# Optimization experiments

Hardware: AMD Instinct MI355X
Metric: run time of the kernel (lower is better)

The kernel has to match this reference:

```python
import jax, jax.numpy as jnp
import numpy as np

B, N, D, H, DH = 1, 1024, 512, 16, 32
NBINS, KIT = 68, 20
NEG = jnp.float32(-1e9)


def _ln(x, g, b):
    mu = jnp.mean(x, -1, keepdims=True)
    var = jnp.mean((x - mu) ** 2, -1, keepdims=True)
    return (x - mu) * jax.lax.rsqrt(var + 1e-5) * g + b


def _heads(x, W):
    b, n, _ = x.shape
    return (x @ W).reshape(b, n, H, DH).transpose(0, 2, 1, 3)  # (B,H,N,DH)


def _forward(h, x_res, pos_bins, mask, ln_mha_g, ln_mha_b, w_q, w_k, w_v, w_g, w_o,
             pos_w, ln_ff_g, ln_ff_b, sw_w1, sw_w3, sw_w2, ln_sink_g, ln_sink_b,
             w_q_sink, w_k_sink, alpha_h, r_h, eps, ln_gate_g, ln_gate_b,
             w_gate_w, w_gate_b, lambda_h_raw):
    b, n, d = h.shape
    mcol = mask[:, None, None, :] > 0  # key-side mask (B,1,1,N)
    mrow = mask[:, None, :, None] > 0

    # ---- MHA with positional bias (flash_diff_attn reference math) ----
    h_n = _ln(h, ln_mha_g, ln_mha_b)
    Q = _heads(h_n, w_q)
    K = _heads(h_n, w_k)
    V = _heads(h_n, w_v)
    G = h_n @ w_g  # (B,N,D) gate, per-head view is equivalent flattened
    bias = pos_w[pos_bins].transpose(0, 3, 1, 2)  # (B,N,N,H) -> (B,H,N,N)
    logits = jnp.einsum('bhnd,bhmd->bhnm', Q, K) / np.float32(np.sqrt(DH)) + bias
    logits = jnp.where(mcol, logits, NEG)
    P = jax.nn.softmax(logits, axis=-1)
    att = jnp.einsum('bhnm,bhmd->bhnd', P, V).transpose(0, 2, 1, 3).reshape(b, n, d)
    h = h + jax.nn.sigmoid(G) * (att @ w_o) * mask[..., None]

    # ---- SwiGLU FFN ----
    h_f = _ln(h, ln_ff_g, ln_ff_b)
    ff = (jax.nn.silu(h_f @ sw_w1) * (h_f @ sw_w3)) @ sw_w2
    h = h + ff * mask[..., None]

    # ---- Balanced Sinkhorn OT transport over coordinates ----
    h_s = _ln(h, ln_sink_g, ln_sink_b)
    Qs = _heads(h_s, w_q_sink)
    Ks = _heads(h_s, w_k_sink)
    Qs = Qs / jnp.clip(jnp.linalg.norm(Qs, axis=-1, keepdims=True), 1e-12)
    Ks = Ks / jnp.clip(jnp.linalg.norm(Ks, axis=-1, keepdims=True), 1e-12)
    sim = jnp.einsum('bhnd,bhmd->bhnm', Qs, Ks)  # cosine similarity
    # Gibbs log-kernel: higher (r_h*sim + alpha_h) => lower cost, scaled by per-head eps
    logKmat = (r_h[:, None, None] * sim + alpha_h[:, None, None]) / eps[:, None, None]
    logKmat = jnp.where(mcol, logKmat, NEG)
    logKmat = jnp.where(mrow, logKmat, NEG)
    n_valid = jnp.sum(mask, -1, keepdims=True)  # (B,1)
    log_a = jnp.where(mask > 0, -jnp.log(n_valid), NEG)[:, None, :]  # (B,1,N) uniform marginal

    def sink_step(carry, _):
        f, g = carry
        f = log_a - jax.nn.logsumexp(logKmat + g[..., None, :], axis=-1)
        g = log_a - jax.nn.logsumexp(logKmat + f[..., None], axis=-2)
        return (f, g), None

    f0 = jnp.zeros((b, H, n), h.dtype)
    (f, g), _ = jax.lax.scan(sink_step, (f0, f0), None, length=KIT)
    logP = f[..., None] + logKmat + g[..., None, :]
    Pn = jax.nn.softmax(logP, axis=-1)  # barycentric row-normalized plan
    x_cent = jnp.einsum('bhnm,bmc->bhnc', Pn, x_res)  # (B,H,N,3)
    vec_h = x_cent - x_res[:, None]

    gate = jax.nn.sigmoid(_ln(h, ln_gate_g, ln_gate_b) @ w_gate_w + w_gate_b)  # (B,N,1)
    lam = (jnp.tanh(lambda_h_raw) / H).reshape(1, H, 1, 1)
    disp = jnp.sum(lam * vec_h, axis=1)  # (B,N,3)
    x_out = x_res + gate * disp * mask[..., None]
    return h, x_out


def setup_inputs() -> dict:
    key = jax.random.key(0)
    ks = jax.random.split(key, 16)
    w = lambda k, s: (0.02 * jax.random.normal(k, s)).astype(jnp.float32)
    nr = H // 4
    return {
        'h': jax.random.normal(ks[0], (B, N, D), jnp.float32),
        'x_res': jax.random.normal(ks[1], (B, N, 3), jnp.float32),
        'pos_bins': jax.random.randint(ks[2], (B, N, N), 0, NBINS),
        'mask': jnp.ones((B, N), jnp.float32),
        'ln_mha_g': jnp.ones(D), 'ln_mha_b': jnp.zeros(D),
        'w_q': w(ks[3], (D, D)), 'w_k': w(ks[4], (D, D)), 'w_v': w(ks[5], (D, D)),
        'w_g': w(ks[6], (D, D)), 'w_o': w(ks[7], (D, D)),
        'pos_w': w(ks[8], (NBINS, H)),
        'ln_ff_g': jnp.ones(D), 'ln_ff_b': jnp.zeros(D),
        'sw_w1': w(ks[9], (D, 4 * D)), 'sw_w3': w(ks[10], (D, 4 * D)),
        'sw_w2': w(ks[11], (4 * D, D)),
        'ln_sink_g': jnp.ones(D), 'ln_sink_b': jnp.zeros(D),
        'w_q_sink': w(ks[12], (D, D)), 'w_k_sink': w(ks[13], (D, D)),
        'alpha_h': jnp.full((H,), -1.0, jnp.float32),
        'r_h': jnp.full((H,), 10.0, jnp.float32),
        'eps': jnp.asarray([0.5] * nr + [1.0] * nr + [2.0] * nr + [4.0] * nr, jnp.float32),
        'ln_gate_g': jnp.ones(D), 'ln_gate_b': jnp.zeros(D),
        'w_gate_w': w(ks[14], (D, 1)), 'w_gate_b': jnp.zeros(1),
        'lambda_h_raw': jnp.zeros(H, jnp.float32),
    }


def reference(h, x_res, pos_bins, mask, ln_mha_g, ln_mha_b, w_q, w_k, w_v, w_g, w_o,
              pos_w, ln_ff_g, ln_ff_b, sw_w1, sw_w3, sw_w2, ln_sink_g, ln_sink_b,
              w_q_sink, w_k_sink, alpha_h, r_h, eps, ln_gate_g, ln_gate_b,
              w_gate_w, w_gate_b, lambda_h_raw):
    return _forward(h, x_res, pos_bins, mask, ln_mha_g, ln_mha_b, w_q, w_k, w_v, w_g,
                    w_o, pos_w, ln_ff_g, ln_ff_b, sw_w1, sw_w3, sw_w2, ln_sink_g,
                    ln_sink_b, w_q_sink, w_k_sink, alpha_h, r_h, eps, ln_gate_g,
                    ln_gate_b, w_gate_w, w_gate_b, lambda_h_raw)
```

## Files before the change

### kernel.cpp

```cpp
#include <hip/hip_runtime.h>
#include <hip/hip_bf16.h>
#include <hip/hip_fp16.h>
#include <math.h>

#define NTOK 1024
#define DMODEL 512
#define NHEAD 16
#define DHEAD 32
#define DFF 2048
#define NBINS 68
#define KIT 20
#define NEGV (-1e9f)
#define NEGH (-30000.0f)

typedef __attribute__((ext_vector_type(8))) short bf16x8;
typedef __attribute__((ext_vector_type(4))) float f32x4;
typedef __attribute__((ext_vector_type(8))) unsigned short u16x8;

__device__ inline unsigned short f2bf(float f) {
    unsigned int u = __float_as_uint(f);
    unsigned int r = (u + 0x7fff + ((u >> 16) & 1)) >> 16;
    return (unsigned short)r;
}

__device__ inline float wave_max64(float v) {
    #pragma unroll
    for (int s = 32; s; s >>= 1) v = fmaxf(v, __shfl_xor(v, s, 64));
    return v;
}
__device__ inline float wave_sum64(float v) {
    #pragma unroll
    for (int s = 32; s; s >>= 1) v += __shfl_xor(v, s, 64);
    return v;
}

__global__ void prep_kernel(const float* __restrict__ w_q, const float* __restrict__ w_k,
                            const float* __restrict__ w_v, const float* __restrict__ w_g,
                            const float* __restrict__ w_o, const float* __restrict__ w_qs,
                            const float* __restrict__ w_ks, const float* __restrict__ sw1,
                            const float* __restrict__ sw3, const float* __restrict__ sw2,
                            unsigned short* __restrict__ wt_qkvg, unsigned short* __restrict__ wt_o,
                            unsigned short* __restrict__ wt_qsks, unsigned short* __restrict__ wt_13,
                            unsigned short* __restrict__ wt_2,
                            const float* __restrict__ mask, float* __restrict__ la,
                            float* __restrict__ gv,
                            const float* __restrict__ hin, const float* __restrict__ lng,
                            const float* __restrict__ lnb, unsigned short* __restrict__ hnb) {
    __shared__ float red[256];
    __shared__ float T[32][33];
    int b = blockIdx.x, tid = threadIdx.x;
    if (b == 4864) {
        red[tid] = mask[tid] + mask[tid + 256] + mask[tid + 512] + mask[tid + 768];
        __syncthreads();
        for (int off = 128; off; off >>= 1) { if (tid < off) red[tid] += red[tid + off]; __syncthreads(); }
        float lognv = __logf(red[0]);
        for (int i = tid; i < NTOK; i += 256) la[i] = (mask[i] > 0.f) ? -lognv : NEGV;
        for (int i = tid; i < NHEAD * NTOK; i += 256)
            gv[i] = (mask[i & 1023] > 0.f) ? 0.f : NEGV;
        return;
    }
    if (b > 4864) {
        int n = b - 4865;
        const float* row = hin + (size_t)n * DMODEL;
        float a = row[tid], bb = row[tid + 256];
        red[tid] = a + bb;
        __syncthreads();
        for (int off = 128; off; off >>= 1) { if (tid < off) red[tid] += red[tid + off]; __syncthreads(); }
        float mu = red[0] * (1.0f / DMODEL);
        __syncthreads();
        float d0 = a - mu, d1 = bb - mu;
        red[tid] = d0 * d0 + d1 * d1;
        __syncthreads();
        for (int off = 128; off; off >>= 1) { if (tid < off) red[tid] += red[tid + off]; __syncthreads(); }
        float rstd = rsqrtf(red[0] * (1.0f / DMODEL) + 1e-5f);
        hnb[(size_t)n * DMODEL + tid]       = f2bf(d0 * rstd * lng[tid] + lnb[tid]);
        hnb[(size_t)n * DMODEL + tid + 256] = f2bf(d1 * rstd * lng[tid + 256] + lnb[tid + 256]);
        return;
    }
    const float* W; unsigned short* D; int K, N, t;
    if (b < 1792) {
        int which = b >> 8; t = b & 255; K = 512; N = 512;
        switch (which) {
            case 0: W = w_q;  D = wt_qkvg; break;
            case 1: W = w_k;  D = wt_qkvg + 512 * 512; break;
            case 2: W = w_v;  D = wt_qkvg + 2 * 512 * 512; break;
            case 3: W = w_g;  D = wt_qkvg + 3 * 512 * 512; break;
            case 4: W = w_o;  D = wt_o; break;
            case 5: W = w_qs; D = wt_qsks; break;
            default: W = w_ks; D = wt_qsks + 512 * 512; break;
        }
    } else if (b < 2816) { W = sw1; D = wt_13;              K = 512;  N = 2048; t = b - 1792; }
    else if (b < 3840)   { W = sw3; D = wt_13 + 2048 * 512; K = 512;  N = 2048; t = b - 2816; }
    else                 { W = sw2; D = wt_2;               K = 2048; N = 512;  t = b - 3840; }
    int nx = N >> 5;
    int n0 = (t % nx) * 32, k0 = (t / nx) * 32;
    int r = tid >> 3, c0 = (tid & 7) * 4;
    float4 v4 = *(const float4*)&W[(size_t)(k0 + r) * N + n0 + c0];
    T[r][c0] = v4.x; T[r][c0 + 1] = v4.y; T[r][c0 + 2] = v4.z; T[r][c0 + 3] = v4.w;
    __syncthreads();
    ushort4 o;
    o.x = f2bf(T[c0][r]); o.y = f2bf(T[c0 + 1][r]);
    o.z = f2bf(T[c0 + 2][r]); o.w = f2bf(T[c0 + 3][r]);
    *(ushort4*)&D[(size_t)(n0 + r) * K + k0 + c0] = o;
}

template<int GATED>
__global__ void res_ln_kernel(const float* __restrict__ base, const __half* __restrict__ Gh,
                              const float* __restrict__ t1, const float* __restrict__ mask,
                              const float* __restrict__ gm, const float* __restrict__ bt,
                              float* __restrict__ hout, unsigned short* __restrict__ lnout) {
    int n = blockIdx.x, tid = threadIdx.x;
    __shared__ float red[256];
    float mk = mask[n];
    size_t off = (size_t)n * DMODEL;
    float a, b;
    if (GATED) {
        float g0 = __half2float(Gh[off + tid]);
        float g1 = __half2float(Gh[off + tid + 256]);
        a = base[off + tid]       + g0 * t1[off + tid]       * mk;
        b = base[off + tid + 256] + g1 * t1[off + tid + 256] * mk;
    } else {
        a = base[off + tid]       + t1[off + tid]       * mk;
        b = base[off + tid + 256] + t1[off + tid + 256] * mk;
    }
    hout[off + tid] = a; hout[off + tid + 256] = b;
    red[tid] = a + b;
    __syncthreads();
    for (int o2 = 128; o2; o2 >>= 1) { if (tid < o2) red[tid] += red[tid + o2]; __syncthreads(); }
    float mu = red[0] * (1.0f / DMODEL);
    __syncthreads();
    float d0 = a - mu, d1 = b - mu;
    red[tid] = d0 * d0 + d1 * d1;
    __syncthreads();
    for (int o2 = 128; o2; o2 >>= 1) { if (tid < o2) red[tid] += red[tid + o2]; __syncthreads(); }
    float rstd = rsqrtf(red[0] * (1.0f / DMODEL) + 1e-5f);
    lnout[off + tid]       = f2bf(d0 * rstd * gm[tid] + bt[tid]);
    lnout[off + tid + 256] = f2bf(d1 * rstd * gm[tid + 256] + bt[tid + 256]);
}

template<int MODE>
__global__ __launch_bounds__(256)
void mfma_gemm(const unsigned short* __restrict__ A, const unsigned short* __restrict__ Bt,
               float* __restrict__ C, __half* __restrict__ Ch, unsigned short* __restrict__ Cb,
               unsigned short* __restrict__ P2, unsigned short* __restrict__ P3,
               int N, int K, int lda, int ldb, int ldc,
               long sA, long sB, long sC) {
    __shared__ unsigned short As[128 * 64];
    __shared__ unsigned short Bs[128 * 64];
    int h = blockIdx.z;
    A += (size_t)h * sA; Bt += (size_t)h * sB;
    const int tid = threadIdx.x;
    const int lane = tid & 63, wid = tid >> 6;
    const int wr = wid >> 1, wc = wid & 1;
    const int lr = lane & 15, kg = lane >> 4;
    const int row0 = blockIdx.y * 128, col0 = blockIdx.x * 128;
    f32x4 acc[4][4];
    #pragma unroll
    for (int i = 0; i < 4; i++)
        #pragma unroll
        for (int j = 0; j < 4; j++) acc[i][j] = (f32x4){0.f, 0.f, 0.f, 0.f};

    for (int k0 = 0; k0 < K; k0 += 64) {
        #pragma unroll
        for (int i = 0; i < 4; i++) {
            int cid = tid + i * 256;
            int r = cid >> 3, sl = cid & 7;
            int rb = col0 + r; if (rb > N - 1) rb = N - 1;
            u16x8 va = *(const u16x8*)&A[(size_t)(row0 + r) * lda + k0 + sl * 8];
            u16x8 vb = *(const u16x8*)&Bt[(size_t)rb * ldb + k0 + sl * 8];
            *(u16x8*)&As[r * 64 + ((sl ^ (r & 7)) * 8)] = va;
            *(u16x8*)&Bs[r * 64 + ((sl ^ (r & 7)) * 8)] = vb;
        }
        __syncthreads();
        #pragma unroll
        for (int ks = 0; ks < 2; ks++) {
            bf16x8 af[4], bfr[4];
            #pragma unroll
            for (int f = 0; f < 4; f++) {
                int ra = wr * 64 + f * 16 + lr;
                af[f] = *(const bf16x8*)&As[ra * 64 + (((ks * 4 + kg) ^ (ra & 7)) * 8)];
                int rb = wc * 64 + f * 16 + lr;
                bfr[f] = *(const bf16x8*)&Bs[rb * 64 + (((ks * 4 + kg) ^ (rb & 7)) * 8)];
            }
            #pragma unroll
            for (int i = 0; i < 4; i++)
                #pragma unroll
                for (int j = 0; j < 4; j++)
                    acc[i][j] = __builtin_amdgcn_mfma_f32_16x16x32_bf16(af[i], bfr[j], acc[i][j], 0, 0, 0);
        }
        __syncthreads();
    }
    #pragma unroll
    for (int i = 0; i < 4; i++) {
        int row = row0 + wr * 64 + i * 16 + kg * 4;
        #pragma unroll
        for (int j = 0; j < 4; j++) {
            int col = col0 + wc * 64 + j * 16 + lr;
            #pragma unroll
            for (int e = 0; e < 4; e++) {
                float v = acc[i][j][e];
                if (MODE == 0) {
                    C[(size_t)h * sC + (size_t)(row + e) * ldc + col] = v;
                } else if (MODE == 2) {
                    if (col < N)
                        Cb[(size_t)h * sC + (size_t)(row + e) * ldc + col] = f2bf(v);
                } else if (MODE == 3) {
                    Ch[(size_t)h * sC + (size_t)(row + e) * ldc + col] = __float2half(v);
                } else {
                    int region = col >> 9;
                    int cc = col & 511;
                    int hh = cc >> 5, kk = cc & 31;
                    if (region == 0) {
                        size_t bidx = (((size_t)hh << 10) + (row + e)) * 64 + kk;
                        Cb[bidx] = f2bf(v * 0.17677669529663687f);
                        Cb[bidx + 32] = 0;
                    } else if (region == 1) {
                        size_t bidx = (((size_t)hh << 10) + (row + e)) * 64 + kk;
                        P2[bidx] = f2bf(v);
                        P2[bidx + 32] = 0;
                    } else if (region == 2) {
                        P3[(((size_t)hh * 32 + kk) << 10) + (row + e)] = f2bf(v);
                    } else {
                        Ch[(size_t)(row + e) * 512 + cc] = __float2half(1.f / (1.f + __expf(-v)));
                    }
                }
            }
        }
    }
}

__global__ __launch_bounds__(256)
void ffn13_gemm(const unsigned short* __restrict__ A, const unsigned short* __restrict__ B1,
                const unsigned short* __restrict__ B2, unsigned short* __restrict__ outb) {
    __shared__ unsigned short As[128 * 64];
    __shared__ unsigned short B1s[128 * 64];
    __shared__ unsigned short B2s[128 * 64];
    const int tid = threadIdx.x;
    const int lane = tid & 63, wid = tid >> 6;
    const int wr = wid >> 1, wc = wid & 1;
    const int lr = lane & 15, kg = lane >> 4;
    const int row0 = blockIdx.y * 128, col0 = blockIdx.x * 128;
    f32x4 acc1[4][4], acc2[4][4];
    #pragma unroll
    for (int i = 0; i < 4; i++)
        #pragma unroll
        for (int j = 0; j < 4; j++) { acc1[i][j] = (f32x4){0,0,0,0}; acc2[i][j] = (f32x4){0,0,0,0}; }
    for (int k0 = 0; k0 < 512; k0 += 64) {
        #pragma unroll
        for (int i = 0; i < 4; i++) {
            int cid = tid + i * 256;
            int r = cid >> 3, sl = cid & 7;
            u16x8 va = *(const u16x8*)&A[(size_t)(row0 + r) * 512 + k0 + sl * 8];
            u16x8 v1 = *(const u16x8*)&B1[(size_t)(col0 + r) * 512 + k0 + sl * 8];
            u16x8 v2 = *(const u16x8*)&B2[(size_t)(col0 + r) * 512 + k0 + sl * 8];
            *(u16x8*)&As[r * 64 + ((sl ^ (r & 7)) * 8)] = va;
            *(u16x8*)&B1s[r * 64 + ((sl ^ (r & 7)) * 8)] = v1;
            *(u16x8*)&B2s[r * 64 + ((sl ^ (r & 7)) * 8)] = v2;
        }
        __syncthreads();
        #pragma unroll
        for (int ks = 0; ks < 2; ks++) {
            bf16x8 af[4], b1f[4], b2f[4];
            #pragma unroll
            for (int f = 0; f < 4; f++) {
                int ra = wr * 64 + f * 16 + lr;
                af[f] = *(const bf16x8*)&As[ra * 64 + (((ks * 4 + kg) ^ (ra & 7)) * 8)];
                int rb = wc * 64 + f * 16 + lr;
                b1f[f] = *(const bf16x8*)&B1s[rb * 64 + (((ks * 4 + kg) ^ (rb & 7)) * 8)];
                b2f[f] = *(const bf16x8*)&B2s[rb * 64 + (((ks * 4 + kg) ^ (rb & 7)) * 8)];
            }
            #pragma unroll
            for (int i = 0; i < 4; i++)
                #pragma unroll
                for (int j = 0; j < 4; j++) {
                    acc1[i][j] = __builtin_amdgcn_mfma_f32_16x16x32_bf16(af[i], b1f[j], acc1[i][j], 0, 0, 0);
                    acc2[i][j] = __builtin_amdgcn_mfma_f32_16x16x32_bf16(af[i], b2f[j], acc2[i][j], 0, 0, 0);
                }
        }
        __syncthreads();
    }
    #pragma unroll
    for (int i = 0; i < 4; i++) {
        int row = row0 + wr * 64 + i * 16 + kg * 4;
        #pragma unroll
        for (int j = 0; j < 4; j++) {
            int col = col0 + wc * 64 + j * 16 + lr;
            #pragma unroll
            for (int e = 0; e < 4; e++) {
                float x = acc1[i][j][e], y = acc2[i][j][e];
                outb[(size_t)(row + e) * 2048 + col] = f2bf(x / (1.f + __expf(-x)) * y);
            }
        }
    }
}

__global__ __launch_bounds__(256)
void bias_softmax_kernel(__half* __restrict__ S, const int* __restrict__ pos_bins,
                         const float* __restrict__ pos_w, const float* __restrict__ mask) {
    __shared__ int   bins_s[NTOK];
    __shared__ float pw_s[NBINS * NHEAD];
    int n = blockIdx.x, tid = threadIdx.x;
    int lane = tid & 63, wid = tid >> 6;
    #pragma unroll
    for (int i = 0; i < 4; i++) {
        int m = tid + i * 256;
        int b = pos_bins[(size_t)n * NTOK + m];
        bins_s[m] = (mask[m] > 0.f) ? b : -1;
    }
    #pragma unroll
    for (int i = 0; i < 5; i++) {
        int idx = tid + i * 256;
        if (idx < NBINS * NHEAD) pw_s[idx] = pos_w[idx];
    }
    __syncthreads();
    int mb = lane * 16;
    #pragma unroll
    for (int hh = 0; hh < 4; hh++) {
        int h = wid * 4 + hh;
        __half* row = S + ((size_t)h * NTOK + n) * NTOK;
        uint4 ua = ((const uint4*)row)[lane * 2];
        uint4 ub = ((const uint4*)row)[lane * 2 + 1];
        unsigned uu[8] = {ua.x, ua.y, ua.z, ua.w, ub.x, ub.y, ub.z, ub.w};
        float v[16];
        #pragma unroll
        for (int j = 0; j < 8; j++) {
            float2 f = __half22float2(*(__half2*)&uu[j]);
            v[2 * j] = f.x; v[2 * j + 1] = f.y;
        }
        float mx = -INFINITY;
        #pragma unroll
        for (int j = 0; j < 16; j++) {
            int b = bins_s[mb + j];
            v[j] = (b >= 0) ? v[j] + pw_s[b * NHEAD + h] : NEGV;
            mx = fmaxf(mx, v[j]);
        }
        mx = wave_max64(mx);
        float sum = 0.f;
        #pragma unroll
        for (int j = 0; j < 16; j++) { v[j] = __expf(v[j] - mx); sum += v[j]; }
        float inv = 1.f / wave_sum64(sum);
        unsigned short o[16];
        #pragma unroll
        for (int j = 0; j < 16; j++) o[j] = f2bf(v[j] * inv);
        ((uint4*)row)[lane * 2]     = *(uint4*)&o[0];
        ((uint4*)row)[lane * 2 + 1] = *(uint4*)&o[8];
    }
}

__global__ void norm_pad_kernel(const float* __restrict__ qsks, const float* __restrict__ rh,
                                const float* __restrict__ ev,
                                unsigned short* __restrict__ Qsc, unsigned short* __restrict__ Ksc) {
    int idx = blockIdx.x * 256 + threadIdx.x;
    int h = idx >> 10, n = idx & 1023;
    const float* q = &qsks[(size_t)n * 1024 + h * 32];
    const float* k = q + 512;
    float s = rh[h] / ev[h];
    float qv[32], kv[32];
    float ssq = 0.f, ssk = 0.f;
    #pragma unroll
    for (int d = 0; d < 32; d++) {
        qv[d] = q[d]; ssq += qv[d] * qv[d];
        kv[d] = k[d]; ssk += kv[d] * kv[d];
    }
    float iq = s / fmaxf(sqrtf(ssq), 1e-12f);
    float ik = 1.f / fmaxf(sqrtf(ssk), 1e-12f);
    size_t base = (size_t)idx * 32;
    #pragma unroll
    for (int d = 0; d < 32; d++) {
        Qsc[base + d] = f2bf(qv[d] * iq);
        Ksc[base + d] = f2bf(kv[d] * ik);
    }
}

template<int TRANSPORT>
__global__ __launch_bounds__(256)
void sink_fused_kernel(const unsigned short* __restrict__ Arows,
                       const unsigned short* __restrict__ Bcols,
                       const float* __restrict__ dual, const float* __restrict__ frow,
                       const float* __restrict__ la,
                       const float* __restrict__ alpha, const float* __restrict__ epsv,
                       const float* __restrict__ x_res,
                       float* __restrict__ outv, float* __restrict__ xc) {
    __shared__ float part[4][16][4];
    const int tid = threadIdx.x, lane = tid & 63, w = tid >> 6;
    const int b = blockIdx.x;
    const int h = b >> 6, row0 = (b & 63) << 4;
    const float bet = alpha[h] / epsv[h];
    const size_t hb = (size_t)h << 10;
    bf16x8 af = *(const bf16x8*)&Arows[(hb + row0 + (lane & 15)) * 32 + (lane >> 4) * 8];
    float fr[4];
    if (TRANSPORT) {
        float4 f4 = *(const float4*)&frow[hb + row0 + (lane >> 4) * 4];
        fr[0] = f4.x; fr[1] = f4.y; fr[2] = f4.z; fr[3] = f4.w;
    }
    const int wbase = w << 8;
    float s[4] = {0.f, 0.f, 0.f, 0.f};
    float a0[4] = {0.f, 0.f, 0.f, 0.f}, a1[4] = {0.f, 0.f, 0.f, 0.f}, a2[4] = {0.f, 0.f, 0.f, 0.f};
    #pragma unroll
    for (int t = 0; t < 16; t++) {
        int col = wbase + t * 16 + (lane & 15);
        bf16x8 bf = *(const bf16x8*)&Bcols[(hb + col) * 32 + (lane >> 4) * 8];
        f32x4 acc = (f32x4){0.f, 0.f, 0.f, 0.f};
        acc = __builtin_amdgcn_mfma_f32_16x16x32_bf16(af, bf, acc, 0, 0, 0);
        float gcol = dual[hb + col];
        float x0, x1, x2;
        if (TRANSPORT) {
            const float* xr = x_res + col * 3;
            x0 = xr[0]; x1 = xr[1]; x2 = xr[2];
        }
        #pragma unroll
        for (int e = 0; e < 4; e++) {
            float v = acc[e] + bet + gcol;
            if (TRANSPORT) v += fr[e];
            float ev = __expf(v);
            s[e] += ev;
            if (TRANSPORT) { a0[e] += ev * x0; a1[e] += ev * x1; a2[e] += ev * x2; }
        }
    }
    #pragma unroll
    for (int off = 1; off < 16; off <<= 1) {
        #pragma unroll
        for (int e = 0; e < 4; e++) {
            s[e] += __shfl_xor(s[e], off, 64);
            if (TRANSPORT) {
                a0[e] += __shfl_xor(a0[e], off, 64);
                a1[e] += __shfl_xor(a1[e], off, 64);
                a2[e] += __shfl_xor(a2[e], off, 64);
            }
        }
    }
    if ((lane & 15) == 0) {
        int rg = (lane >> 4) * 4;
        #pragma unroll
        for (int e = 0; e < 4; e++) {
            part[w][rg + e][0] = s[e];
            if (TRANSPORT) {
                part[w][rg + e][1] = a0[e];
                part[w][rg + e][2] = a1[e];
                part[w][rg + e][3] = a2[e];
            }
        }
    }
    __syncthreads();
    if (tid < 16) {
        float tot = part[0][tid][0] + part[1][tid][0] + part[2][tid][0] + part[3][tid][0];
        int row = row0 + tid;
        if (!TRANSPORT) {
            outv[hb + row] = la[row] - __logf(fmaxf(tot, 1e-38f));
        } else {
            float inv = 1.f / fmaxf(tot, 1e-38f);
            float b0 = part[0][tid][1] + part[1][tid][1] + part[2][tid][1] + part[3][tid][1];
            float b1 = part[0][tid][2] + part[1][tid][2] + part[2][tid][2] + part[3][tid][2];
            float b2 = part[0][tid][3] + part[1][tid][3] + part[2][tid][3] + part[3][tid][3];
            xc[(hb + row) * 3 + 0] = b0 * inv;
            xc[(hb + row) * 3 + 1] = b1 * inv;
            xc[(hb + row) * 3 + 2] = b2 * inv;
        }
    }
}

__global__ void final_kernel(const float* __restrict__ h2, const float* __restrict__ x_res,
                             const float* __restrict__ mask, const float* __restrict__ gm,
                             const float* __restrict__ bt, const float* __restrict__ wg,
                             const float* __restrict__ wb, const float* __restrict__ lamraw,
                             const float* __restrict__ xc, float* __restrict__ xout) {
    int n = blockIdx.x;
    int tid = threadIdx.x;
    __shared__ float red[256];
    const float* row = h2 + (size_t)n * DMODEL;
    float a = row[tid], b = row[tid + 256];
    red[tid] = a + b;
    __syncthreads();
    for (int off = 128; off; off >>= 1) { if (tid < off) red[tid] += red[tid + off]; __syncthreads(); }
    float mu = red[0] * (1.0f / DMODEL);
    __syncthreads();
    float d0 = a - mu, d1 = b - mu;
    red[tid] = d0 * d0 + d1 * d1;
    __syncthreads();
    for (int off = 128; off; off >>= 1) { if (tid < off) red[tid] += red[tid + off]; __syncthreads(); }
    float rstd = rsqrtf(red[0] * (1.0f / DMODEL) + 1e-5f);
    __syncthreads();
    float t0 = (d0 * rstd * gm[tid] + bt[tid]) * wg[tid];
    float t1 = (d1 * rstd * gm[tid + 256] + bt[tid + 256]) * wg[tid + 256];
    red[tid] = t0 + t1;
    __syncthreads();
    for (int off = 128; off; off >>= 1) { if (tid < off) red[tid] += red[tid + off]; __syncthreads(); }
    if (tid == 0) {
        float gate = 1.f / (1.f + expf(-(red[0] + wb[0])));
        float mk = mask[n];
        #pragma unroll
        for (int c = 0; c < 3; c++) {
            float xr = x_res[n * 3 + c];
            float disp = 0.f;
            for (int h = 0; h < NHEAD; h++) {
                float lam = tanhf(lamraw[h]) * (1.f / NHEAD);
                disp += lam * (xc[((size_t)h * NTOK + n) * 3 + c] - xr);
            }
            xout[n * 3 + c] = xr + gate * disp * mk;
        }
    }
}

extern "C" void kernel_launch(void* const* d_in, const int* in_sizes, int n_in,
                              void* d_out, int out_size, void* d_ws, size_t ws_size,
                              hipStream_t stream) {
    const float* h          = (const float*)d_in[0];
    const float* x_res      = (const float*)d_in[1];
    const int*   pos_bins   = (const int*)d_in[2];
    const float* mask       = (const float*)d_in[3];
    const float* ln_mha_g   = (const float*)d_in[4];
    const float* ln_mha_b   = (const float*)d_in[5];
    const float* w_q        = (const float*)d_in[6];
    const float* w_k        = (const float*)d_in[7];
    const float* w_v        = (const float*)d_in[8];
    const float* w_g        = (const float*)d_in[9];
    const float* w_o        = (const float*)d_in[10];
    const float* pos_w      = (const float*)d_in[11];
    const float* ln_ff_g    = (const float*)d_in[12];
    const float* ln_ff_b    = (const float*)d_in[13];
    const float* sw_w1      = (const float*)d_in[14];
    const float* sw_w3      = (const float*)d_in[15];
    const float* sw_w2      = (const float*)d_in[16];
    const float* ln_sink_g  = (const float*)d_in[17];
    const float* ln_sink_b  = (const float*)d_in[18];
    const float* w_q_sink   = (const float*)d_in[19];
    const float* w_k_sink   = (const float*)d_in[20];
    const float* alpha_h    = (const float*)d_in[21];
    const float* r_h        = (const float*)d_in[22];
    const float* eps        = (const float*)d_in[23];
    const float* ln_gate_g  = (const float*)d_in[24];
    const float* ln_gate_b  = (const float*)d_in[25];
    const float* w_gate_w   = (const float*)d_in[26];
    const float* w_gate_b   = (const float*)d_in[27];
    const float* lambda_raw = (const float*)d_in[28];
    float* out = (float*)d_out;
    const size_t ND = (size_t)NTOK * DMODEL;

    char* Wp = (char*)d_ws;
    auto alloc = [&](size_t bytes) { char* p = Wp; Wp += (bytes + 255) & ~(size_t)255; return p; };
    unsigned short* wt_qkvg = (unsigned short*)alloc((size_t)2048 * 512 * 2);
    unsigned short* wt_o    = (unsigned short*)alloc((size_t)512 * 512 * 2);
    unsigned short* wt_13   = (unsigned short*)alloc((size_t)4096 * 512 * 2);
    unsigned short* wt_2    = (unsigned short*)alloc((size_t)512 * 2048 * 2);
    unsigned short* wt_qsks = (unsigned short*)alloc((size_t)1024 * 512 * 2);
    unsigned short* hnb     = (unsigned short*)alloc(ND * 2);
    __half*         Gh      = (__half*)alloc(ND * 2);
    unsigned short* attb    = (unsigned short*)alloc(ND * 2);
    float*          t1      = (float*)alloc(ND * 4);
    float*          h1      = (float*)alloc(ND * 4);
    unsigned short* ffb     = (unsigned short*)alloc((size_t)1024 * 2048 * 2);
    unsigned short* Qp      = (unsigned short*)alloc((size_t)16 * 1024 * 64 * 2);
    unsigned short* Kp      = (unsigned short*)alloc((size_t)16 * 1024 * 64 * 2);
    unsigned short* Vt      = (unsigned short*)alloc((size_t)16 * 32 * 1024 * 2);
    unsigned short* Qsc     = (unsigned short*)alloc((size_t)16 * 1024 * 32 * 2);
    unsigned short* Ksc     = (unsigned short*)alloc((size_t)16 * 1024 * 32 * 2);
    float*          qsks    = (float*)alloc((size_t)1024 * 1024 * 4);
    char*           R       = alloc((size_t)32 * 1024 * 1024);
    float*          fv      = (float*)alloc((size_t)16 * 1024 * 4);
    float*          gv      = (float*)alloc((size_t)16 * 1024 * 4);
    float*          la      = (float*)alloc((size_t)1024 * 4);
    float*          xc      = (float*)alloc((size_t)16 * 1024 * 3 * 4);

    __half* Sh_att = (__half*)R;

    prep_kernel<<<5889, 256, 0, stream>>>(w_q, w_k, w_v, w_g, w_o, w_q_sink, w_k_sink,
                                          sw_w1, sw_w3, sw_w2,
                                          wt_qkvg, wt_o, wt_qsks, wt_13, wt_2,
                                          mask, la, gv,
                                          h, ln_mha_g, ln_mha_b, hnb);

    mfma_gemm<4><<<dim3(16, 8, 1), 256, 0, stream>>>(hnb, wt_qkvg, nullptr, Gh, Qp, Kp, Vt,
        2048, 512, 512, 512, 2048, 0, 0, 0);
    mfma_gemm<3><<<dim3(8, 8, 16), 256, 0, stream>>>(Qp, Kp, nullptr, Sh_att, nullptr, nullptr, nullptr,
        1024, 64, 64, 64, 1024, 65536, 65536, 1048576);
    bias_softmax_kernel<<<NTOK, 256, 0, stream>>>(Sh_att, pos_bins, pos_w, mask);
    mfma_gemm<2><<<dim3(1, 8, 16), 256, 0, stream>>>((const unsigned short*)Sh_att, Vt,
        nullptr, nullptr, attb, nullptr, nullptr,
        32, 1024, 1024, 1024, 512, 1048576, 32768, 32);
    mfma_gemm<0><<<dim3(4, 8, 1), 256, 0, stream>>>(attb, wt_o, t1, nullptr, nullptr, nullptr, nullptr,
        512, 512, 512, 512, 512, 0, 0, 0);
    res_ln_kernel<1><<<NTOK, 256, 0, stream>>>(h, Gh, t1, mask, ln_ff_g, ln_ff_b, h1, hnb);

    ffn13_gemm<<<dim3(16, 8), 256, 0, stream>>>(hnb, wt_13, wt_13 + 2048 * 512, ffb);
    mfma_gemm<0><<<dim3(4, 8, 1), 256, 0, stream>>>(ffb, wt_2, t1, nullptr, nullptr, nullptr, nullptr,
        512, 2048, 2048, 2048, 512, 0, 0, 0);
    res_ln_kernel<0><<<NTOK, 256, 0, stream>>>(h1, nullptr, t1, mask, ln_sink_g, ln_sink_b, out, hnb);

    mfma_gemm<0><<<dim3(8, 8, 1), 256, 0, stream>>>(hnb, wt_qsks, qsks, nullptr, nullptr, nullptr, nullptr,
        1024, 512, 512, 512, 1024, 0, 0, 0);
    norm_pad_kernel<<<64, 256, 0, stream>>>(qsks, r_h, eps, Qsc, Ksc);

    for (int it = 0; it < KIT; it++) {
        sink_fused_kernel<0><<<1024, 256, 0, stream>>>(Qsc, Ksc, gv, nullptr, la,
                                                       alpha_h, eps, nullptr, fv, nullptr);
        sink_fused_kernel<0><<<1024, 256, 0, stream>>>(Ksc, Qsc, fv, nullptr, la,
                                                       alpha_h, eps, nullptr, gv, nullptr);
    }
    sink_fused_kernel<1><<<1024, 256, 0, stream>>>(Qsc, Ksc, gv, fv, la,
                                                   alpha_h, eps, x_res, nullptr, xc);

    final_kernel<<<NTOK, 256, 0, stream>>>(out, x_res, mask, ln_gate_g, ln_gate_b,
                                           w_gate_w, w_gate_b, lambda_raw, xc, out + ND);
}
```

Measured before the change: 607.2 us.

## Fuse Q/K norm into sinkhorn GEMM, split-K out-proj/FFN2, move gate LN earlier

Q/K-sink normalization and bf16 packing now run in the projection GEMM epilogue via cross-lane shuffles, which removes the fp32 qsks buffer and the norm_pad kernel. The output-projection and FFN-down GEMMs are split into two K-halves over blockIdx.z, doubling block count for these small-grid GEMMs. The residual+LN kernel sums the two partials. The gate LayerNorm and sigmoid are computed inside the second residual LN kernel, so final_kernel shrinks to a small elementwise pass. This costs extra partial-sum traffic and some extra reduction syncs.

```diff
diff --git a/kernel.cpp b/kernel.cpp
--- a/kernel.cpp
+++ b/kernel.cpp
@@ -11,7 +11,6 @@
 #define NBINS 68
 #define KIT 20
 #define NEGV (-1e9f)
-#define NEGH (-30000.0f)
 
 typedef __attribute__((ext_vector_type(8))) short bf16x8;
 typedef __attribute__((ext_vector_type(4))) float f32x4;
@@ -104,24 +103,30 @@
     *(ushort4*)&D[(size_t)(n0 + r) * K + k0 + c0] = o;
 }
 
-template<int GATED>
+template<int GATED, int GATECALC>
 __global__ void res_ln_kernel(const float* __restrict__ base, const __half* __restrict__ Gh,
-                              const float* __restrict__ t1, const float* __restrict__ mask,
+                              const float* __restrict__ t1a, const float* __restrict__ t1b,
+                              const float* __restrict__ mask,
                               const float* __restrict__ gm, const float* __restrict__ bt,
-                              float* __restrict__ hout, unsigned short* __restrict__ lnout) {
+                              const float* __restrict__ gg, const float* __restrict__ gb,
+                              const float* __restrict__ wg, const float* __restrict__ wb,
+                              float* __restrict__ hout, unsigned short* __restrict__ lnout,
+                              float* __restrict__ gate) {
     int n = blockIdx.x, tid = threadIdx.x;
     __shared__ float red[256];
     float mk = mask[n];
     size_t off = (size_t)n * DMODEL;
+    float s0 = t1a[off + tid] + t1b[off + tid];
+    float s1 = t1a[off + tid + 256] + t1b[off + tid + 256];
     float a, b;
     if (GATED) {
         float g0 = __half2float(Gh[off + tid]);
         float g1 = __half2float(Gh[off + tid + 256]);
-        a = base[off + tid]       + g0 * t1[off + tid]       * mk;
-        b = base[off + tid + 256] + g1 * t1[off + tid + 256] * mk;
+        a = base[off + tid]       + g0 * s0 * mk;
+        b = base[off + tid + 256] + g1 * s1 * mk;
     } else {
-        a = base[off + tid]       + t1[off + tid]       * mk;
-        b = base[off + tid + 256] + t1[off + tid + 256] * mk;
+        a = base[off + tid]       + s0 * mk;
+        b = base[off + tid + 256] + s1 * mk;
     }
     hout[off + tid] = a; hout[off + tid + 256] = b;
     red[tid] = a + b;
@@ -136,6 +141,15 @@
     float rstd = rsqrtf(red[0] * (1.0f / DMODEL) + 1e-5f);
     lnout[off + tid]       = f2bf(d0 * rstd * gm[tid] + bt[tid]);
     lnout[off + tid + 256] = f2bf(d1 * rstd * gm[tid + 256] + bt[tid + 256]);
+    if (GATECALC) {
+        float t0 = (d0 * rstd * gg[tid] + gb[tid]) * wg[tid];
+        float t1v = (d1 * rstd * gg[tid + 256] + gb[tid + 256]) * wg[tid + 256];
+        __syncthreads();
+        red[tid] = t0 + t1v;
+        __syncthreads();
+        for (int o2 = 128; o2; o2 >>= 1) { if (tid < o2) red[tid] += red[tid + o2]; __syncthreads(); }
+        if (tid == 0) gate[n] = 1.f / (1.f + expf(-(red[0] + wb[0])));
+    }
 }
 
 template<int MODE>
@@ -144,7 +158,8 @@
                float* __restrict__ C, __half* __restrict__ Ch, unsigned short* __restrict__ Cb,
                unsigned short* __restrict__ P2, unsigned short* __restrict__ P3,
                int N, int K, int lda, int ldb, int ldc,
-               long sA, long sB, long sC) {
+               long sA, long sB, long sC,
+               const float* __restrict__ rh, const float* __restrict__ ev) {
     __shared__ unsigned short As[128 * 64];
     __shared__ unsigned short Bs[128 * 64];
     int h = blockIdx.z;
@@ -189,6 +204,40 @@
                     acc[i][j] = __builtin_amdgcn_mfma_f32_16x16x32_bf16(af[i], bfr[j], acc[i][j], 0, 0, 0);
         }
         __syncthreads();
+    }
+    if (MODE == 6) {
+        #pragma unroll
+        for (int i = 0; i < 4; i++) {
+            int row = row0 + wr * 64 + i * 16 + kg * 4;
+            #pragma unroll
+            for (int jp = 0; jp < 2; jp++) {
+                int j0 = jp * 2, j1 = j0 + 1;
+                int colbase = col0 + wc * 64 + j0 * 16;
+                bool isQ = colbase < 512;
+                int hh = (colbase & 511) >> 5;
+                float ss[4];
+                #pragma unroll
+                for (int e = 0; e < 4; e++) {
+                    float v0 = acc[i][j0][e], v1 = acc[i][j1][e];
+                    float t = v0 * v0 + v1 * v1;
+                    t += __shfl_xor(t, 1, 64);
+                    t += __shfl_xor(t, 2, 64);
+                    t += __shfl_xor(t, 4, 64);
+                    t += __shfl_xor(t, 8, 64);
+                    ss[e] = t;
+                }
+                float sc = isQ ? (rh[hh] / ev[hh]) : 1.f;
+                unsigned short* D = isQ ? Cb : P2;
+                #pragma unroll
+                for (int e = 0; e < 4; e++) {
+                    float inv = sc / fmaxf(sqrtf(ss[e]), 1e-12f);
+                    size_t rbase = (((size_t)hh << 10) + row + e) * 32;
+                    D[rbase + lr]      = f2bf(acc[i][j0][e] * inv);
+                    D[rbase + 16 + lr] = f2bf(acc[i][j1][e] * inv);
+                }
+            }
+        }
+        return;
     }
     #pragma unroll
     for (int i = 0; i < 4; i++) {
@@ -347,31 +396,6 @@
     }
 }
 
-__global__ void norm_pad_kernel(const float* __restrict__ qsks, const float* __restrict__ rh,
-                                const float* __restrict__ ev,
-                                unsigned short* __restrict__ Qsc, unsigned short* __restrict__ Ksc) {
-    int idx = blockIdx.x * 256 + threadIdx.x;
-    int h = idx >> 10, n = idx & 1023;
-    const float* q = &qsks[(size_t)n * 1024 + h * 32];
-    const float* k = q + 512;
-    float s = rh[h] / ev[h];
-    float qv[32], kv[32];
-    float ssq = 0.f, ssk = 0.f;
-    #pragma unroll
-    for (int d = 0; d < 32; d++) {
-        qv[d] = q[d]; ssq += qv[d] * qv[d];
-        kv[d] = k[d]; ssk += kv[d] * kv[d];
-    }
-    float iq = s / fmaxf(sqrtf(ssq), 1e-12f);
-    float ik = 1.f / fmaxf(sqrtf(ssk), 1e-12f);
-    size_t base = (size_t)idx * 32;
-    #pragma unroll
-    for (int d = 0; d < 32; d++) {
-        Qsc[base + d] = f2bf(qv[d] * iq);
-        Ksc[base + d] = f2bf(kv[d] * ik);
-    }
-}
-
 template<int TRANSPORT>
 __global__ __launch_bounds__(256)
 void sink_fused_kernel(const unsigned short* __restrict__ Arows,
@@ -459,45 +483,23 @@
     }
 }
 
-__global__ void final_kernel(const float* __restrict__ h2, const float* __restrict__ x_res,
-                             const float* __restrict__ mask, const float* __restrict__ gm,
-                             const float* __restrict__ bt, const float* __restrict__ wg,
-                             const float* __restrict__ wb, const float* __restrict__ lamraw,
+__global__ void final_kernel(const float* __restrict__ x_res, const float* __restrict__ mask,
+                             const float* __restrict__ lamraw, const float* __restrict__ gate,
                              const float* __restrict__ xc, float* __restrict__ xout) {
-    int n = blockIdx.x;
+    __shared__ float lam[NHEAD];
     int tid = threadIdx.x;
-    __shared__ float red[256];
-    const float* row = h2 + (size_t)n * DMODEL;
-    float a = row[tid], b = row[tid + 256];
-    red[tid] = a + b;
+    if (tid < NHEAD) lam[tid] = tanhf(lamraw[tid]) * (1.f / NHEAD);
     __syncthreads();
-    for (int off = 128; off; off >>= 1) { if (tid < off) red[tid] += red[tid + off]; __syncthreads(); }
-    float mu = red[0] * (1.0f / DMODEL);
-    __syncthreads();
-    float d0 = a - mu, d1 = b - mu;
-    red[tid] = d0 * d0 + d1 * d1;
-    __syncthreads();
-    for (int off = 128; off; off >>= 1) { if (tid < off) red[tid] += red[tid + off]; __syncthreads(); }
-    float rstd = rsqrtf(red[0] * (1.0f / DMODEL) + 1e-5f);
-    __syncthreads();
-    float t0 = (d0 * rstd * gm[tid] + bt[tid]) * wg[tid];
-    float t1 = (d1 * rstd * gm[tid + 256] + bt[tid + 256]) * wg[tid + 256];
-    red[tid] = t0 + t1;
-    __syncthreads();
-    for (int off = 128; off; off >>= 1) { if (tid < off) red[tid] += red[tid + off]; __syncthreads(); }
-    if (tid == 0) {
-        float gate = 1.f / (1.f + expf(-(red[0] + wb[0])));
-        float mk = mask[n];
-        #pragma unroll
-        for (int c = 0; c < 3; c++) {
-            float xr = x_res[n * 3 + c];
-            float disp = 0.f;
-            for (int h = 0; h < NHEAD; h++) {
-                float lam = tanhf(lamraw[h]) * (1.f / NHEAD);
-                disp += lam * (xc[((size_t)h * NTOK + n) * 3 + c] - xr);
-            }
-            xout[n * 3 + c] = xr + gate * disp * mk;
-        }
+    int n = blockIdx.x * 256 + tid;
+    float g = gate[n] * mask[n];
+    #pragma unroll
+    for (int c = 0; c < 3; c++) {
+        float xr = x_res[n * 3 + c];
+        float disp = 0.f;
+        #pragma unroll
+        for (int h = 0; h < NHEAD; h++)
+            disp += lam[h] * (xc[(((size_t)h << 10) + n) * 3 + c] - xr);
+        xout[n * 3 + c] = xr + g * disp;
     }
 }
 
@@ -546,7 +548,7 @@
     unsigned short* hnb     = (unsigned short*)alloc(ND * 2);
     __half*         Gh      = (__half*)alloc(ND * 2);
     unsigned short* attb    = (unsigned short*)alloc(ND * 2);
-    float*          t1      = (float*)alloc(ND * 4);
+    float*          t1      = (float*)alloc(ND * 4 * 2);
     float*          h1      = (float*)alloc(ND * 4);
     unsigned short* ffb     = (unsigned short*)alloc((size_t)1024 * 2048 * 2);
     unsigned short* Qp      = (unsigned short*)alloc((size_t)16 * 1024 * 64 * 2);
@@ -554,12 +556,12 @@
     unsigned short* Vt      = (unsigned short*)alloc((size_t)16 * 32 * 1024 * 2);
     unsigned short* Qsc     = (unsigned short*)alloc((size_t)16 * 1024 * 32 * 2);
     unsigned short* Ksc     = (unsigned short*)alloc((size_t)16 * 1024 * 32 * 2);
-    float*          qsks    = (float*)alloc((size_t)1024 * 1024 * 4);
     char*           R       = alloc((size_t)32 * 1024 * 1024);
     float*          fv      = (float*)alloc((size_t)16 * 1024 * 4);
     float*          gv      = (float*)alloc((size_t)16 * 1024 * 4);
     float*          la      = (float*)alloc((size_t)1024 * 4);
     float*          xc      = (float*)alloc((size_t)16 * 1024 * 3 * 4);
+    float*          gate    = (float*)alloc((size_t)1024 * 4);
 
     __half* Sh_att = (__half*)R;
 
@@ -570,25 +572,26 @@
                                           h, ln_mha_g, ln_mha_b, hnb);
 
     mfma_gemm<4><<<dim3(16, 8, 1), 256, 0, stream>>>(hnb, wt_qkvg, nullptr, Gh, Qp, Kp, Vt,
-        2048, 512, 512, 512, 2048, 0, 0, 0);
+        2048, 512, 512, 512, 2048, 0, 0, 0, nullptr, nullptr);
     mfma_gemm<3><<<dim3(8, 8, 16), 256, 0, stream>>>(Qp, Kp, nullptr, Sh_att, nullptr, nullptr, nullptr,
-        1024, 64, 64, 64, 1024, 65536, 65536, 1048576);
+        1024, 64, 64, 64, 1024, 65536, 65536, 1048576, nullptr, nullptr);
     bias_softmax_kernel<<<NTOK, 256, 0, stream>>>(Sh_att, pos_bins, pos_w, mask);
     mfma_gemm<2><<<dim3(1, 8, 16), 256, 0, stream>>>((const unsigned short*)Sh_att, Vt,
         nullptr, nullptr, attb, nullptr, nullptr,
-        32, 1024, 1024, 1024, 512, 1048576, 32768, 32);
-    mfma_gemm<0><<<dim3(4, 8, 1), 256, 0, stream>>>(attb, wt_o, t1, nullptr, nullptr, nullptr, nullptr,
-        512, 512, 512, 512, 512, 0, 0, 0);
-    res_ln_kernel<1><<<NTOK, 256, 0, stream>>>(h, Gh, t1, mask, ln_ff_g, ln_ff_b, h1, hnb);
+        32, 1024, 1024, 1024, 512, 1048576, 32768, 32, nullptr, nullptr);
+    mfma_gemm<0><<<dim3(4, 8, 2), 256, 0, stream>>>(attb, wt_o, t1, nullptr, nullptr, nullptr, nullptr,
+        512, 256, 512, 512, 512, 256, 256, (long)ND, nullptr, nullptr);
+    res_ln_kernel<1, 0><<<NTOK, 256, 0, stream>>>(h, Gh, t1, t1 + ND, mask, ln_ff_g, ln_ff_b,
+        nullptr, nullptr, nullptr, nullptr, h1, hnb, nullptr);
 
     ffn13_gemm<<<dim3(16, 8), 256, 0, stream>>>(hnb, wt_13, wt_13 + 2048 * 512, ffb);
-    mfma_gemm<0><<<dim3(4, 8, 1), 256, 0, stream>>>(ffb, wt_2, t1, nullptr, nullptr, nullptr, nullptr,
-        512, 2048, 2048, 2048, 512, 0, 0, 0);
-    res_ln_kernel<0><<<NTOK, 256, 0, stream>>>(h1, nullptr, t1, mask, ln_sink_g, ln_sink_b, out, hnb);
-
-    mfma_gemm<0><<<dim3(8, 8, 1), 256, 0, stream>>>(hnb, wt_qsks, qsks, nullptr, nullptr, nullptr, nullptr,
-        1024, 512, 512, 512, 1024, 0, 0, 0);
-    norm_pad_kernel<<<64, 256, 0, stream>>>(qsks, r_h, eps, Qsc, Ksc);
+    mfma_gemm<0><<<dim3(4, 8, 2), 256, 0, stream>>>(ffb, wt_2, t1, nullptr, nullptr, nullptr, nullptr,
+        512, 1024, 2048, 2048, 512, 1024, 1024, (long)ND, nullptr, nullptr);
+    res_ln_kernel<0, 1><<<NTOK, 256, 0, stream>>>(h1, nullptr, t1, t1 + ND, mask, ln_sink_g, ln_sink_b,
+        ln_gate_g, ln_gate_b, w_gate_w, w_gate_b, out, hnb, gate);
+
+    mfma_gemm<6><<<dim3(8, 8, 1), 256, 0, stream>>>(hnb, wt_qsks, nullptr, nullptr, Qsc, Ksc, nullptr,
+        1024, 512, 512, 512, 1024, 0, 0, 0, r_h, eps);
 
     for (int it = 0; it < KIT; it++) {
         sink_fused_kernel<0><<<1024, 256, 0, stream>>>(Qsc, Ksc, gv, nullptr, la,
@@ -599,6 +602,5 @@
     sink_fused_kernel<1><<<1024, 256, 0, stream>>>(Qsc, Ksc, gv, fv, la,
                                                    alpha_h, eps, x_res, nullptr, xc);
 
-    final_kernel<<<NTOK, 256, 0, stream>>>(out, x_res, mask, ln_gate_g, ln_gate_b,
-                                           w_gate_w, w_gate_b, lambda_raw, xc, out + ND);
-}
+    final_kernel<<<4, 256, 0, stream>>>(x_res, mask, lambda_raw, gate, xc, out + ND);
+}
```

Measured after the change: 574.0 us. -5.5%, faster.
